# Performance work log

Hardware: AMD Instinct MI355X
Metric: run time of the kernel (lower is better)

Reference implementation:

```python
import jax, jax.numpy as jnp
import numpy as np


def setup_inputs() -> dict:
    key = jax.random.key(0)
    ks = jax.random.split(key, 6)
    B, S, I, H = 8, 4096, 512, 512
    scale = 1.0 / np.sqrt(I)
    return {
        "x": jax.random.normal(ks[0], (B, S, I), dtype=jnp.float32),
        "h_0": jax.random.normal(ks[1], (B, H), dtype=jnp.float32),
        "W_z": jax.random.normal(ks[2], (H, I), dtype=jnp.float32) * scale,
        "b_z": jax.random.normal(ks[3], (H,), dtype=jnp.float32) * scale,
        "W_h": jax.random.normal(ks[4], (H, I), dtype=jnp.float32) * scale,
        "b_h": jax.random.normal(ks[5], (H,), dtype=jnp.float32) * scale,
    }


def reference(x, h_0, W_z, b_z, W_h, b_h):
    # Gate and candidate projections (dense GEMMs over all timesteps at once)
    z = jax.nn.sigmoid(jnp.einsum("bsi,hi->bsh", x, W_z) + b_z)  # [B,S,H]
    h_tilde = jnp.einsum("bsi,hi->bsh", x, W_h) + b_h            # [B,S,H]

    # Linear recurrence h_t = a_t * h_{t-1} + b_t with a = 1-z, b = z*h_tilde.
    # Parallel associative scan over time; h_0 folded in as element 0 (a=1, b=h_0).
    a = jnp.concatenate([jnp.ones_like(h_0)[:, None, :], 1.0 - z], axis=1)     # [B,S+1,H]
    b = jnp.concatenate([h_0[:, None, :], z * h_tilde], axis=1)                # [B,S+1,H]

    def combine(c1, c2):
        a1, b1 = c1
        a2, b2 = c2
        return a1 * a2, a2 * b1 + b2

    _, h = jax.lax.associative_scan(combine, (a, b), axis=1)
    return h[:, 1:, :]  # drop the h_0 slot -> [B,S,H]
```

## Files before the change

kernel.cpp:

```cpp
#include <hip/hip_runtime.h>
#include <hip/hip_bf16.h>
#include <stdint.h>


typedef __attribute__((ext_vector_type(8))) short short8;
typedef __attribute__((ext_vector_type(4))) float f32x4;

#define AS1 __attribute__((address_space(1)))
#define AS3 __attribute__((address_space(3)))

__device__ inline void gload_lds16(const void* g, void* l) {
  __builtin_amdgcn_global_load_lds((AS1 uint32_t*)(g), (AS3 uint32_t*)(l), 16, 0, 0);
}

__device__ inline ushort f2bf(float f) {
  union { __hip_bfloat16 h; ushort u; } v;
  v.h = __float2bfloat16(f);
  return v.u;
}

__global__ void cvt_all(const float* __restrict__ x,
                        const float* __restrict__ wz,
                        const float* __restrict__ wh,
                        ushort* __restrict__ xb,
                        ushort* __restrict__ wzb,
                        ushort* __restrict__ whb) {
  int i = blockIdx.x * 256 + threadIdx.x;
  for (; i < 4325376; i += 2048 * 256) {
    const float* s; ushort* d; int j;
    if (i < 4194304)      { s = x;  d = xb;  j = i; }
    else if (i < 4259840) { s = wz; d = wzb; j = i - 4194304; }
    else                  { s = wh; d = whb; j = i - 4259840; }
    float4 v = reinterpret_cast<const float4*>(s)[j];
    ushort4 o = make_ushort4(f2bf(v.x), f2bf(v.y), f2bf(v.z), f2bf(v.w));
    reinterpret_cast<ushort4*>(d)[j] = o;
  }
}

__global__ __launch_bounds__(256, 2) void gemm_gate(
    const ushort* __restrict__ xb,
    const ushort* __restrict__ wzb,
    const ushort* __restrict__ whb,
    const float* __restrict__ b_z,
    const float* __restrict__ b_h,
    uint* __restrict__ ab,
    float2* __restrict__ ABc)
{
  __shared__ __align__(16) char smem[73728];

  const int t  = threadIdx.x;
  const int w  = t >> 6;
  const int l  = t & 63;
  const int lm = l & 15;
  const int lk = l >> 4;
  const int wm = w >> 1, wn = w & 1;
  const int bid  = blockIdx.x;
  const int tile = (bid & 7) * 128 + (bid >> 3);
  const int bx = tile >> 2;
  const int by = tile & 3;
  const int m0 = bx * 128;
  const int n0 = by * 128;

  const int srow = t >> 2;
  const int ssl  = t & 3;

  f32x4 acc[2][4][4];
  #pragma unroll
  for (int q = 0; q < 2; ++q)
    #pragma unroll
    for (int m = 0; m < 4; ++m)
      #pragma unroll
      for (int n = 0; n < 4; ++n)
        acc[q][m][n] = (f32x4){0.f, 0.f, 0.f, 0.f};

  auto stage = [&](int sel, int kt) {
    char* base = smem + sel * 24576;
    const int k0 = kt * 32;
    #pragma unroll
    for (int j = 0; j < 2; ++j) {
      int row = j * 64 + srow;
      int gs  = ssl ^ ((row >> 1) & 3);
      gload_lds16(xb + (size_t)(m0 + row) * 512 + k0 + gs * 8,
                  base + j * 4096 + w * 1024);
      gload_lds16(wzb + (size_t)(n0 + row) * 512 + k0 + gs * 8,
                  base + 8192 + j * 4096 + w * 1024);
      gload_lds16(whb + (size_t)(n0 + row) * 512 + k0 + gs * 8,
                  base + 16384 + j * 4096 + w * 1024);
    }
  };

  stage(0, 0);
  stage(1, 1);

  #pragma unroll
  for (int kt = 0; kt < 16; ++kt) {
    const int sel = kt % 3;
    if (kt < 14) {
      stage((kt + 2) % 3, kt + 2);
      asm volatile("s_waitcnt vmcnt(12)" ::: "memory");
    } else if (kt == 14) {
      asm volatile("s_waitcnt vmcnt(6)" ::: "memory");
    } else {
      asm volatile("s_waitcnt vmcnt(0)" ::: "memory");
    }
    __builtin_amdgcn_s_barrier();

    const char* base = smem + sel * 24576;
    short8 af[4], bfz[4], bfh[4];
    #pragma unroll
    for (int m = 0; m < 4; ++m) {
      int row = wm * 64 + m * 16 + lm;
      af[m] = *(const short8*)(base + row * 64 + ((lk ^ ((row >> 1) & 3)) << 4));
    }
    #pragma unroll
    for (int n = 0; n < 4; ++n) {
      int row = wn * 64 + n * 16 + lm;
      int so  = ((lk ^ ((row >> 1) & 3)) << 4);
      bfz[n] = *(const short8*)(base + 8192  + row * 64 + so);
      bfh[n] = *(const short8*)(base + 16384 + row * 64 + so);
    }
    __builtin_amdgcn_s_setprio(1);
    #pragma unroll
    for (int m = 0; m < 4; ++m)
      #pragma unroll
      for (int n = 0; n < 4; ++n) {
        acc[0][m][n] = __builtin_amdgcn_mfma_f32_16x16x32_bf16(af[m], bfz[n], acc[0][m][n], 0, 0, 0);
        acc[1][m][n] = __builtin_amdgcn_mfma_f32_16x16x32_bf16(af[m], bfh[n], acc[1][m][n], 0, 0, 0);
      }
    __builtin_amdgcn_s_setprio(0);
    __builtin_amdgcn_s_barrier();
  }

  #pragma unroll
  for (int n = 0; n < 4; ++n) {
    const int col = n0 + wn * 64 + n * 16 + lm;
    const float bzn = b_z[col];
    const float bhn = b_h[col];
    float av[4][4], bv[4][4];
    #pragma unroll
    for (int m = 0; m < 4; ++m) {
      #pragma unroll
      for (int j = 0; j < 4; ++j) {
        size_t grow = (size_t)(m0 + wm * 64 + m * 16 + lk * 4 + j);
        float uz = acc[0][m][n][j] + bzn;
        float uh = acc[1][m][n][j] + bhn;
        float z  = 1.f / (1.f + __expf(-uz));
        float a  = 1.f - z;
        float bb = z * uh;
        av[m][j] = a;
        bv[m][j] = bb;
        ab[grow * 512 + n0 + wn * 64 + n * 16 + lm] =
            (uint)f2bf(a) | ((uint)f2bf(bb) << 16);
      }
    }
    #pragma unroll
    for (int cb = 0; cb < 2; ++cb) {
      float At[2], Bt[2];
      #pragma unroll
      for (int mm = 0; mm < 2; ++mm) {
        float A = 1.f, Bv = 0.f;
        #pragma unroll
        for (int j = 0; j < 4; ++j) {
          float a = av[2 * cb + mm][j];
          float b = bv[2 * cb + mm][j];
          A  = a * A;
          Bv = a * Bv + b;
        }
        float Ag = 1.f, Bg = 0.f;
        #pragma unroll
        for (int q = 0; q < 4; ++q) {
          float Aq = __shfl(A,  lm + 16 * q);
          float Bq = __shfl(Bv, lm + 16 * q);
          Ag = Aq * Ag;
          Bg = Aq * Bg + Bq;
        }
        At[mm] = Ag;
        Bt[mm] = Bg;
      }
      float Achunk = At[1] * At[0];
      float Bchunk = At[1] * Bt[0] + Bt[1];
      if (lk == 0) {
        int bidx = bx >> 5;
        int c    = (bx & 31) * 4 + wm * 2 + cb;
        ABc[((size_t)bidx * 512 + col) * 128 + c] = make_float2(Achunk, Bchunk);
      }
    }
  }
}

__global__ __launch_bounds__(256) void chunk_scan(
    const float2* __restrict__ ABc,
    const float* __restrict__ h0,
    float* __restrict__ Hinit)
{
  __shared__ float sm[128][4];
  const int w = threadIdx.x >> 6, l = threadIdx.x & 63;
  const int b   = blockIdx.x >> 7;
  const int h0g = (blockIdx.x & 127) * 4;
  const int h   = h0g + w;

  const float2* base = ABc + ((size_t)b * 512 + h) * 128;
  float2 s1 = base[l];
  float2 s2 = base[64 + l];

  float A1 = s1.x, B1 = s1.y;
  #pragma unroll
  for (int d = 1; d < 64; d <<= 1) {
    float uA = __shfl_up(A1, d);
    float uB = __shfl_up(B1, d);
    if (l >= d) { B1 = A1 * uB + B1; A1 = A1 * uA; }
  }
  float A2 = s2.x, B2 = s2.y;
  #pragma unroll
  for (int d = 1; d < 64; d <<= 1) {
    float uA = __shfl_up(A2, d);
    float uB = __shfl_up(B2, d);
    if (l >= d) { B2 = A2 * uB + B2; A2 = A2 * uA; }
  }
  float PA = __shfl(A1, 63), PB = __shfl(B1, 63);
  float FA = A2 * PA;
  float FB = A2 * PB + B2;

  float e1A = __shfl_up(A1, 1), e1B = __shfl_up(B1, 1);
  if (l == 0) { e1A = 1.f; e1B = 0.f; }
  float e2A = __shfl_up(FA, 1), e2B = __shfl_up(FB, 1);
  if (l == 0) { e2A = PA; e2B = PB; }

  float h0v = h0[b * 512 + h];
  sm[l][w]      = e1A * h0v + e1B;
  sm[64 + l][w] = e2A * h0v + e2B;
  __syncthreads();

  const int tt = threadIdx.x;
  if (tt < 128) {
    float4 v = *(const float4*)sm[tt];
    *(float4*)(Hinit + ((size_t)b * 128 + tt) * 512 + h0g) = v;
  }
}

__global__ __launch_bounds__(256) void scan_write(
    const uint* __restrict__ ab,
    const float* __restrict__ Hinit,
    float* __restrict__ out)
{
  int tid = blockIdx.x * 256 + threadIdx.x;
  int cg = tid & 127;
  int c  = (tid >> 7) & 127;
  int b  = tid >> 14;
  const uint4* p = reinterpret_cast<const uint4*>(ab + ((size_t)(b * 4096 + c * 32)) * 512) + cg;
  float4 hv = *reinterpret_cast<const float4*>(Hinit + ((size_t)b * 128 + c) * 512 + cg * 4);
  float4* po = reinterpret_cast<float4*>(out + ((size_t)(b * 4096 + c * 32)) * 512) + cg;
  #pragma unroll 4
  for (int t = 0; t < 32; ++t) {
    uint4 u = p[(size_t)t * 128];
    hv.x = __uint_as_float(u.x << 16) * hv.x + __uint_as_float(u.x & 0xffff0000u);
    hv.y = __uint_as_float(u.y << 16) * hv.y + __uint_as_float(u.y & 0xffff0000u);
    hv.z = __uint_as_float(u.z << 16) * hv.z + __uint_as_float(u.z & 0xffff0000u);
    hv.w = __uint_as_float(u.w << 16) * hv.w + __uint_as_float(u.w & 0xffff0000u);
    po[(size_t)t * 128] = hv;
  }
}

extern "C" void kernel_launch(void* const* d_in, const int* in_sizes, int n_in,
                              void* d_out, int out_size, void* d_ws, size_t ws_size,
                              hipStream_t stream) {
  const float* x   = (const float*)d_in[0];
  const float* h0  = (const float*)d_in[1];
  const float* W_z = (const float*)d_in[2];
  const float* b_z = (const float*)d_in[3];
  const float* W_h = (const float*)d_in[4];
  const float* b_h = (const float*)d_in[5];
  float* out = (float*)d_out;

  char* ws = (char*)d_ws;
  ushort* xb    = (ushort*)(ws);
  ushort* wzb   = (ushort*)(ws + 33554432);
  ushort* whb   = (ushort*)(ws + 34078720);
  uint*   ab    = (uint*)  (ws + 34603008);
  float2* ABc   = (float2*)(ws + 101711872);
  float*  Hinit = (float*) (ws + 105906176);

  cvt_all<<<2048, 256, 0, stream>>>(x, W_z, W_h, xb, wzb, whb);
  gemm_gate<<<1024, 256, 0, stream>>>(xb, wzb, whb, b_z, b_h, ab, ABc);
  chunk_scan<<<1024, 256, 0, stream>>>(ABc, h0, Hinit);
  scan_write<<<512, 256, 0, stream>>>(ab, Hinit, out);
}
```

Baseline: 94.55 us.

## Switch gate GEMM to 32x32x16 MFMA and restructure chunk-scan epilogue

Replaces the 16x16x32 bf16 MFMA tiling with 32x32x16 MFMAs over 2x2 accumulator tiles per wave. This cuts the number of LDS fragment loads and MFMA issues per k-step. The pipeline now waits and barriers before issuing the next stage's prefetch, which removes the trailing barrier in each iteration. The epilogue is rewritten for the 32x32 output layout and combines the two row halves with an xor-32 shuffle instead of four broadcast shuffles. This changes register pressure and the order in which the scan is combined.

```diff
diff --git a/kernel.cpp b/kernel.cpp
--- a/kernel.cpp
+++ b/kernel.cpp
@@ -3,8 +3,8 @@
 #include <stdint.h>
 
 
-typedef __attribute__((ext_vector_type(8))) short short8;
-typedef __attribute__((ext_vector_type(4))) float f32x4;
+typedef __attribute__((ext_vector_type(8)))  short short8;
+typedef __attribute__((ext_vector_type(16))) float f32x16;
 
 #define AS1 __attribute__((address_space(1)))
 #define AS3 __attribute__((address_space(3)))
@@ -48,11 +48,11 @@
 {
   __shared__ __align__(16) char smem[73728];
 
-  const int t  = threadIdx.x;
-  const int w  = t >> 6;
-  const int l  = t & 63;
-  const int lm = l & 15;
-  const int lk = l >> 4;
+  const int t   = threadIdx.x;
+  const int w   = t >> 6;
+  const int l   = t & 63;
+  const int c32 = l & 31;
+  const int hi  = l >> 5;
   const int wm = w >> 1, wn = w & 1;
   const int bid  = blockIdx.x;
   const int tile = (bid & 7) * 128 + (bid >> 3);
@@ -64,14 +64,14 @@
   const int srow = t >> 2;
   const int ssl  = t & 3;
 
-  f32x4 acc[2][4][4];
-  #pragma unroll
-  for (int q = 0; q < 2; ++q)
-    #pragma unroll
-    for (int m = 0; m < 4; ++m)
-      #pragma unroll
-      for (int n = 0; n < 4; ++n)
-        acc[q][m][n] = (f32x4){0.f, 0.f, 0.f, 0.f};
+  f32x16 accz[2][2], acch[2][2];
+  #pragma unroll
+  for (int tm = 0; tm < 2; ++tm)
+    #pragma unroll
+    for (int tn = 0; tn < 2; ++tn) {
+      accz[tm][tn] = (f32x16)(0.f);
+      acch[tm][tn] = (f32x16)(0.f);
+    }
 
   auto stage = [&](int sel, int kt) {
     char* base = smem + sel * 24576;
@@ -95,94 +95,92 @@
   #pragma unroll
   for (int kt = 0; kt < 16; ++kt) {
     const int sel = kt % 3;
-    if (kt < 14) {
-      stage((kt + 2) % 3, kt + 2);
-      asm volatile("s_waitcnt vmcnt(12)" ::: "memory");
-    } else if (kt == 14) {
+    if (kt < 15) {
       asm volatile("s_waitcnt vmcnt(6)" ::: "memory");
     } else {
       asm volatile("s_waitcnt vmcnt(0)" ::: "memory");
     }
     __builtin_amdgcn_s_barrier();
+    if (kt < 14) stage((kt + 2) % 3, kt + 2);
 
     const char* base = smem + sel * 24576;
-    short8 af[4], bfz[4], bfh[4];
-    #pragma unroll
-    for (int m = 0; m < 4; ++m) {
-      int row = wm * 64 + m * 16 + lm;
-      af[m] = *(const short8*)(base + row * 64 + ((lk ^ ((row >> 1) & 3)) << 4));
-    }
-    #pragma unroll
-    for (int n = 0; n < 4; ++n) {
-      int row = wn * 64 + n * 16 + lm;
-      int so  = ((lk ^ ((row >> 1) & 3)) << 4);
-      bfz[n] = *(const short8*)(base + 8192  + row * 64 + so);
-      bfh[n] = *(const short8*)(base + 16384 + row * 64 + so);
+    short8 af[2][2], bfz[2][2], bfh[2][2];
+    #pragma unroll
+    for (int tm = 0; tm < 2; ++tm) {
+      int row = wm * 64 + tm * 32 + c32;
+      int rsw = (row >> 1) & 3;
+      #pragma unroll
+      for (int ks = 0; ks < 2; ++ks)
+        af[tm][ks] = *(const short8*)(base + row * 64 + (((ks * 2 + hi) ^ rsw) << 4));
+    }
+    #pragma unroll
+    for (int tn = 0; tn < 2; ++tn) {
+      int row = wn * 64 + tn * 32 + c32;
+      int rsw = (row >> 1) & 3;
+      #pragma unroll
+      for (int ks = 0; ks < 2; ++ks) {
+        int so = (((ks * 2 + hi) ^ rsw) << 4);
+        bfz[tn][ks] = *(const short8*)(base + 8192  + row * 64 + so);
+        bfh[tn][ks] = *(const short8*)(base + 16384 + row * 64 + so);
+      }
     }
     __builtin_amdgcn_s_setprio(1);
     #pragma unroll
-    for (int m = 0; m < 4; ++m)
-      #pragma unroll
-      for (int n = 0; n < 4; ++n) {
-        acc[0][m][n] = __builtin_amdgcn_mfma_f32_16x16x32_bf16(af[m], bfz[n], acc[0][m][n], 0, 0, 0);
-        acc[1][m][n] = __builtin_amdgcn_mfma_f32_16x16x32_bf16(af[m], bfh[n], acc[1][m][n], 0, 0, 0);
+    for (int tm = 0; tm < 2; ++tm)
+      #pragma unroll
+      for (int tn = 0; tn < 2; ++tn) {
+        accz[tm][tn] = __builtin_amdgcn_mfma_f32_32x32x16_bf16(af[tm][0], bfz[tn][0], accz[tm][tn], 0, 0, 0);
+        accz[tm][tn] = __builtin_amdgcn_mfma_f32_32x32x16_bf16(af[tm][1], bfz[tn][1], accz[tm][tn], 0, 0, 0);
+        acch[tm][tn] = __builtin_amdgcn_mfma_f32_32x32x16_bf16(af[tm][0], bfh[tn][0], acch[tm][tn], 0, 0, 0);
+        acch[tm][tn] = __builtin_amdgcn_mfma_f32_32x32x16_bf16(af[tm][1], bfh[tn][1], acch[tm][tn], 0, 0, 0);
       }
     __builtin_amdgcn_s_setprio(0);
-    __builtin_amdgcn_s_barrier();
-  }
-
-  #pragma unroll
-  for (int n = 0; n < 4; ++n) {
-    const int col = n0 + wn * 64 + n * 16 + lm;
-    const float bzn = b_z[col];
-    const float bhn = b_h[col];
-    float av[4][4], bv[4][4];
-    #pragma unroll
-    for (int m = 0; m < 4; ++m) {
-      #pragma unroll
-      for (int j = 0; j < 4; ++j) {
-        size_t grow = (size_t)(m0 + wm * 64 + m * 16 + lk * 4 + j);
-        float uz = acc[0][m][n][j] + bzn;
-        float uh = acc[1][m][n][j] + bhn;
-        float z  = 1.f / (1.f + __expf(-uz));
-        float a  = 1.f - z;
-        float bb = z * uh;
-        av[m][j] = a;
-        bv[m][j] = bb;
-        ab[grow * 512 + n0 + wn * 64 + n * 16 + lm] =
-            (uint)f2bf(a) | ((uint)f2bf(bb) << 16);
-      }
-    }
-    #pragma unroll
-    for (int cb = 0; cb < 2; ++cb) {
-      float At[2], Bt[2];
-      #pragma unroll
-      for (int mm = 0; mm < 2; ++mm) {
+  }
+
+  const int bidx = bx >> 5;
+  #pragma unroll
+  for (int tm = 0; tm < 2; ++tm) {
+    #pragma unroll
+    for (int tn = 0; tn < 2; ++tn) {
+      const int col = n0 + wn * 64 + tn * 32 + c32;
+      const float bzn = b_z[col];
+      const float bhn = b_h[col];
+      float segA[4], segB[4];
+      #pragma unroll
+      for (int q = 0; q < 4; ++q) {
         float A = 1.f, Bv = 0.f;
         #pragma unroll
         for (int j = 0; j < 4; ++j) {
-          float a = av[2 * cb + mm][j];
-          float b = bv[2 * cb + mm][j];
+          const int reg  = q * 4 + j;
+          const int rloc = j + 8 * q + 4 * hi;
+          float uz = accz[tm][tn][reg] + bzn;
+          float uh = acch[tm][tn][reg] + bhn;
+          float z  = 1.f / (1.f + __expf(-uz));
+          float a  = 1.f - z;
+          float bb = z * uh;
+          size_t grow = (size_t)(m0 + wm * 64 + tm * 32 + rloc);
+          ab[grow * 512 + col] = (uint)f2bf(a) | ((uint)f2bf(bb) << 16);
           A  = a * A;
-          Bv = a * Bv + b;
+          Bv = a * Bv + bb;
         }
-        float Ag = 1.f, Bg = 0.f;
-        #pragma unroll
-        for (int q = 0; q < 4; ++q) {
-          float Aq = __shfl(A,  lm + 16 * q);
-          float Bq = __shfl(Bv, lm + 16 * q);
-          Ag = Aq * Ag;
-          Bg = Aq * Bg + Bq;
-        }
-        At[mm] = Ag;
-        Bt[mm] = Bg;
-      }
-      float Achunk = At[1] * At[0];
-      float Bchunk = At[1] * Bt[0] + Bt[1];
-      if (lk == 0) {
-        int bidx = bx >> 5;
-        int c    = (bx & 31) * 4 + wm * 2 + cb;
-        ABc[((size_t)bidx * 512 + col) * 128 + c] = make_float2(Achunk, Bchunk);
+        segA[q] = A;
+        segB[q] = Bv;
+      }
+      float FA = 1.f, FB = 0.f;
+      #pragma unroll
+      for (int q = 0; q < 4; ++q) {
+        float pA = __shfl_xor(segA[q], 32);
+        float pB = __shfl_xor(segB[q], 32);
+        float fA = hi ? pA : segA[q];
+        float fB = hi ? pB : segB[q];
+        float sA = hi ? segA[q] : pA;
+        float sB = hi ? segB[q] : pB;
+        FB = fA * FB + fB; FA = fA * FA;
+        FB = sA * FB + sB; FA = sA * FA;
+      }
+      if (hi == 0) {
+        int c = (bx & 31) * 4 + wm * 2 + tm;
+        ABc[((size_t)bidx * 512 + col) * 128 + c] = make_float2(FA, FB);
       }
     }
   }
```

Result: no change. 95.93 us (+1.5%).

## Use 256x256 GEMM tiles with interleaved W_z/W_h weights and phased pipeline

Applied to the files above, without the earlier changes.

Concatenates W_z and W_h into one interleaved weight matrix during conversion, so each GEMM block computes a 256x256 tile (128 gate and 128 candidate columns) with 512 threads and 128KB LDS. The K loop now uses 64-wide steps with double-buffered A/B regions and a phased schedule that issues loads between MFMA groups. The intent is to raise arithmetic intensity and cut global/LDS traffic per MFMA. The cost is more LDS per block, lower occupancy, and more complex synchronization.

```diff
diff --git a/kernel.cpp b/kernel.cpp
--- a/kernel.cpp
+++ b/kernel.cpp
@@ -23,166 +23,183 @@
                         const float* __restrict__ wz,
                         const float* __restrict__ wh,
                         ushort* __restrict__ xb,
-                        ushort* __restrict__ wzb,
-                        ushort* __restrict__ whb) {
+                        ushort* __restrict__ wcat) {
   int i = blockIdx.x * 256 + threadIdx.x;
   for (; i < 4325376; i += 2048 * 256) {
     const float* s; ushort* d; int j;
-    if (i < 4194304)      { s = x;  d = xb;  j = i; }
-    else if (i < 4259840) { s = wz; d = wzb; j = i - 4194304; }
-    else                  { s = wh; d = whb; j = i - 4259840; }
-    float4 v = reinterpret_cast<const float4*>(s)[j];
-    ushort4 o = make_ushort4(f2bf(v.x), f2bf(v.y), f2bf(v.z), f2bf(v.w));
-    reinterpret_cast<ushort4*>(d)[j] = o;
-  }
-}
-
-__global__ __launch_bounds__(256, 2) void gemm_gate(
+    if (i < 4194304) {
+      s = x; d = xb; j = i;
+      float4 v = reinterpret_cast<const float4*>(s)[j];
+      reinterpret_cast<ushort4*>(d)[j] =
+          make_ushort4(f2bf(v.x), f2bf(v.y), f2bf(v.z), f2bf(v.w));
+    } else {
+      j = i - 4194304;
+      int row = j >> 7, c4 = j & 127;
+      int g = row >> 6, q = row & 63;
+      const float* src = (q < 32) ? (wz + (size_t)(g * 32 + q) * 512)
+                                  : (wh + (size_t)(g * 32 + q - 32) * 512);
+      float4 v = reinterpret_cast<const float4*>(src)[c4];
+      reinterpret_cast<ushort4*>(wcat)[j] =
+          make_ushort4(f2bf(v.x), f2bf(v.y), f2bf(v.z), f2bf(v.w));
+    }
+  }
+}
+
+__global__ __launch_bounds__(512, 2) void gemm_gate(
     const ushort* __restrict__ xb,
-    const ushort* __restrict__ wzb,
-    const ushort* __restrict__ whb,
+    const ushort* __restrict__ wcat,
     const float* __restrict__ b_z,
     const float* __restrict__ b_h,
     uint* __restrict__ ab,
     float2* __restrict__ ABc)
 {
-  __shared__ __align__(16) char smem[73728];
+  __shared__ __align__(16) char smem[131072];
 
   const int t  = threadIdx.x;
   const int w  = t >> 6;
   const int l  = t & 63;
   const int lm = l & 15;
   const int lk = l >> 4;
-  const int wm = w >> 1, wn = w & 1;
+  const int wm = w >> 2;
+  const int wn = w & 3;
+
   const int bid  = blockIdx.x;
-  const int tile = (bid & 7) * 128 + (bid >> 3);
-  const int bx = tile >> 2;
-  const int by = tile & 3;
-  const int m0 = bx * 128;
-  const int n0 = by * 128;
-
-  const int srow = t >> 2;
-  const int ssl  = t & 3;
-
-  f32x4 acc[2][4][4];
-  #pragma unroll
-  for (int q = 0; q < 2; ++q)
+  const int tile = (bid & 7) * 64 + (bid >> 3);
+  const int mt = tile >> 2;
+  const int nt = tile & 3;
+  const int m0 = mt * 256;
+  const int n0 = nt * 256;
+
+  const int sr8 = l >> 3;
+  const int gs  = (l & 7) ^ sr8;
+
+  enum { B0A = 0, B0B = 32768, B1A = 65536, B1B = 98304 };
+
+  f32x4 acc[8][4];
+  #pragma unroll
+  for (int m = 0; m < 8; ++m)
     #pragma unroll
-    for (int m = 0; m < 4; ++m)
-      #pragma unroll
-      for (int n = 0; n < 4; ++n)
-        acc[q][m][n] = (f32x4){0.f, 0.f, 0.f, 0.f};
-
-  auto stage = [&](int sel, int kt) {
-    char* base = smem + sel * 24576;
-    const int k0 = kt * 32;
+    for (int nf = 0; nf < 4; ++nf)
+      acc[m][nf] = (f32x4){0.f, 0.f, 0.f, 0.f};
+
+  auto stageA = [&](int region, int kt, int half) {
     #pragma unroll
     for (int j = 0; j < 2; ++j) {
-      int row = j * 64 + srow;
-      int gs  = ssl ^ ((row >> 1) & 3);
-      gload_lds16(xb + (size_t)(m0 + row) * 512 + k0 + gs * 8,
-                  base + j * 4096 + w * 1024);
-      gload_lds16(wzb + (size_t)(n0 + row) * 512 + k0 + gs * 8,
-                  base + 8192 + j * 4096 + w * 1024);
-      gload_lds16(whb + (size_t)(n0 + row) * 512 + k0 + gs * 8,
-                  base + 16384 + j * 4096 + w * 1024);
+      int row = half * 128 + j * 64 + w * 8 + sr8;
+      gload_lds16(xb + (size_t)(m0 + row) * 512 + kt * 64 + gs * 8,
+                  smem + region + (half * 128 + j * 64) * 128 + w * 1024);
     }
   };
-
-  stage(0, 0);
-  stage(1, 1);
-
-  #pragma unroll
-  for (int kt = 0; kt < 16; ++kt) {
-    const int sel = kt % 3;
-    if (kt < 14) {
-      stage((kt + 2) % 3, kt + 2);
-      asm volatile("s_waitcnt vmcnt(12)" ::: "memory");
-    } else if (kt == 14) {
-      asm volatile("s_waitcnt vmcnt(6)" ::: "memory");
-    } else {
-      asm volatile("s_waitcnt vmcnt(0)" ::: "memory");
+  auto stageB = [&](int region, int kt, int half) {
+    #pragma unroll
+    for (int j = 0; j < 2; ++j) {
+      int row = half * 128 + j * 64 + w * 8 + sr8;
+      gload_lds16(wcat + (size_t)(n0 + row) * 512 + kt * 64 + gs * 8,
+                  smem + region + (half * 128 + j * 64) * 128 + w * 1024);
     }
-    __builtin_amdgcn_s_barrier();
-
-    const char* base = smem + sel * 24576;
-    short8 af[4], bfz[4], bfh[4];
+  };
+
+  short8 aF[2][2], bB[4][2];
+
+#define RD_A(BUFA, MQ)                                                        \
+  _Pragma("unroll") for (int mm = 0; mm < 2; ++mm)                            \
+  _Pragma("unroll") for (int ks = 0; ks < 2; ++ks) {                          \
+    int row = wm * 128 + (2 * (MQ) + mm) * 16 + lm;                           \
+    aF[mm][ks] = *(const short8*)(smem + (BUFA) + row * 128 +                 \
+                                  (((ks * 4 + lk) ^ (lm & 7)) << 4));         \
+  }
+
+#define RD_B(BUFB)                                                            \
+  _Pragma("unroll") for (int nf = 0; nf < 4; ++nf)                            \
+  _Pragma("unroll") for (int ks = 0; ks < 2; ++ks) {                          \
+    int row = wn * 64 + nf * 16 + lm;                                         \
+    bB[nf][ks] = *(const short8*)(smem + (BUFB) + row * 128 +                 \
+                                  (((ks * 4 + lk) ^ (lm & 7)) << 4));         \
+  }
+
+#define PHASE(BUFA, BUFB, MQ, READB, STAGE, VMN)                              \
+  {                                                                           \
+    if (READB) { RD_B(BUFB); }                                                \
+    RD_A(BUFA, MQ);                                                           \
+    STAGE;                                                                    \
+    if ((VMN) == 4)      asm volatile("s_waitcnt vmcnt(4)" ::: "memory");     \
+    else if ((VMN) == 0) asm volatile("s_waitcnt vmcnt(0)" ::: "memory");     \
+    __builtin_amdgcn_s_barrier();                                             \
+    asm volatile("s_waitcnt lgkmcnt(0)" ::: "memory");                        \
+    __builtin_amdgcn_sched_barrier(0);                                        \
+    __builtin_amdgcn_s_setprio(1);                                            \
+    _Pragma("unroll") for (int ks = 0; ks < 2; ++ks)                          \
+    _Pragma("unroll") for (int nf = 0; nf < 4; ++nf) {                        \
+      acc[2 * (MQ)][nf]     = __builtin_amdgcn_mfma_f32_16x16x32_bf16(        \
+          aF[0][ks], bB[nf][ks], acc[2 * (MQ)][nf], 0, 0, 0);                 \
+      acc[2 * (MQ) + 1][nf] = __builtin_amdgcn_mfma_f32_16x16x32_bf16(        \
+          aF[1][ks], bB[nf][ks], acc[2 * (MQ) + 1][nf], 0, 0, 0);             \
+    }                                                                         \
+    __builtin_amdgcn_s_setprio(0);                                            \
+    __builtin_amdgcn_s_barrier();                                             \
+  }
+
+  stageA(B0A, 0, 0); stageA(B0A, 0, 1);
+  stageB(B0B, 0, 0); stageB(B0B, 0, 1);
+  stageB(B1B, 1, 0); stageB(B1B, 1, 1);
+  asm volatile("s_waitcnt vmcnt(4)" ::: "memory");
+  __builtin_amdgcn_s_barrier();
+
+  #pragma unroll
+  for (int it = 0; it < 4; ++it) {
+    const int ko = 2 * it + 1, ke2 = 2 * it + 2, ko2 = 2 * it + 3;
+    PHASE(B0A, B0B, 0, true,  { stageA(B1A, ko, 0); },               -1)
+    PHASE(B0A, B0B, 1, false, { stageA(B1A, ko, 1); },               -1)
+    PHASE(B0A, B0B, 2, false, { if (it < 3) stageB(B0B, ke2, 0); },  -1)
+    PHASE(B0A, B0B, 3, false, { if (it < 3) stageB(B0B, ke2, 1); },  (it < 3) ? 4 : 0)
+    PHASE(B1A, B1B, 0, true,  { if (it < 3) stageA(B0A, ke2, 0); },  -1)
+    PHASE(B1A, B1B, 1, false, { if (it < 3) stageA(B0A, ke2, 1); },  -1)
+    PHASE(B1A, B1B, 2, false, { if (it < 3) stageB(B1B, ko2, 0); },  -1)
+    PHASE(B1A, B1B, 3, false, { if (it < 3) stageB(B1B, ko2, 1); },  (it < 3) ? 4 : 0)
+  }
+#undef PHASE
+#undef RD_A
+#undef RD_B
+
+  const int g    = nt * 4 + wn;
+  const int bidx = mt >> 4;
+  #pragma unroll
+  for (int gp = 0; gp < 2; ++gp) {
+    const int h = g * 32 + gp * 16 + lm;
+    const float bz = b_z[h], bh = b_h[h];
     #pragma unroll
-    for (int m = 0; m < 4; ++m) {
-      int row = wm * 64 + m * 16 + lm;
-      af[m] = *(const short8*)(base + row * 64 + ((lk ^ ((row >> 1) & 3)) << 4));
-    }
-    #pragma unroll
-    for (int n = 0; n < 4; ++n) {
-      int row = wn * 64 + n * 16 + lm;
-      int so  = ((lk ^ ((row >> 1) & 3)) << 4);
-      bfz[n] = *(const short8*)(base + 8192  + row * 64 + so);
-      bfh[n] = *(const short8*)(base + 16384 + row * 64 + so);
-    }
-    __builtin_amdgcn_s_setprio(1);
-    #pragma unroll
-    for (int m = 0; m < 4; ++m)
-      #pragma unroll
-      for (int n = 0; n < 4; ++n) {
-        acc[0][m][n] = __builtin_amdgcn_mfma_f32_16x16x32_bf16(af[m], bfz[n], acc[0][m][n], 0, 0, 0);
-        acc[1][m][n] = __builtin_amdgcn_mfma_f32_16x16x32_bf16(af[m], bfh[n], acc[1][m][n], 0, 0, 0);
-      }
-    __builtin_amdgcn_s_setprio(0);
-    __builtin_amdgcn_s_barrier();
-  }
-
-  #pragma unroll
-  for (int n = 0; n < 4; ++n) {
-    const int col = n0 + wn * 64 + n * 16 + lm;
-    const float bzn = b_z[col];
-    const float bhn = b_h[col];
-    float av[4][4], bv[4][4];
-    #pragma unroll
-    for (int m = 0; m < 4; ++m) {
-      #pragma unroll
-      for (int j = 0; j < 4; ++j) {
-        size_t grow = (size_t)(m0 + wm * 64 + m * 16 + lk * 4 + j);
-        float uz = acc[0][m][n][j] + bzn;
-        float uh = acc[1][m][n][j] + bhn;
-        float z  = 1.f / (1.f + __expf(-uz));
-        float a  = 1.f - z;
-        float bb = z * uh;
-        av[m][j] = a;
-        bv[m][j] = bb;
-        ab[grow * 512 + n0 + wn * 64 + n * 16 + lm] =
-            (uint)f2bf(a) | ((uint)f2bf(bb) << 16);
-      }
-    }
-    #pragma unroll
-    for (int cb = 0; cb < 2; ++cb) {
-      float At[2], Bt[2];
+    for (int cb = 0; cb < 4; ++cb) {
+      float cA = 1.f, cB = 0.f;
       #pragma unroll
       for (int mm = 0; mm < 2; ++mm) {
-        float A = 1.f, Bv = 0.f;
+        const int m = 2 * cb + mm;
+        float sA = 1.f, sB = 0.f;
         #pragma unroll
         for (int j = 0; j < 4; ++j) {
-          float a = av[2 * cb + mm][j];
-          float b = bv[2 * cb + mm][j];
-          A  = a * A;
-          Bv = a * Bv + b;
+          float uz = acc[m][gp][j] + bz;
+          float uh = acc[m][gp + 2][j] + bh;
+          float z  = 1.f / (1.f + __expf(-uz));
+          float a  = 1.f - z;
+          float bb = z * uh;
+          size_t grow = (size_t)(m0 + wm * 128 + m * 16 + lk * 4 + j);
+          ab[grow * 512 + h] = (uint)f2bf(a) | ((uint)f2bf(bb) << 16);
+          sA = a * sA;
+          sB = a * sB + bb;
         }
         float Ag = 1.f, Bg = 0.f;
         #pragma unroll
         for (int q = 0; q < 4; ++q) {
-          float Aq = __shfl(A,  lm + 16 * q);
-          float Bq = __shfl(Bv, lm + 16 * q);
+          float Aq = __shfl(sA, q * 16 + lm);
+          float Bq = __shfl(sB, q * 16 + lm);
           Ag = Aq * Ag;
           Bg = Aq * Bg + Bq;
         }
-        At[mm] = Ag;
-        Bt[mm] = Bg;
+        cB = Ag * cB + Bg;
+        cA = Ag * cA;
       }
-      float Achunk = At[1] * At[0];
-      float Bchunk = At[1] * Bt[0] + Bt[1];
       if (lk == 0) {
-        int bidx = bx >> 5;
-        int c    = (bx & 31) * 4 + wm * 2 + cb;
-        ABc[((size_t)bidx * 512 + col) * 128 + c] = make_float2(Achunk, Bchunk);
+        int c = (mt & 15) * 8 + wm * 4 + cb;
+        ABc[((size_t)bidx * 512 + h) * 128 + c] = make_float2(cA, cB);
       }
     }
   }
@@ -274,14 +291,13 @@
 
   char* ws = (char*)d_ws;
   ushort* xb    = (ushort*)(ws);
-  ushort* wzb   = (ushort*)(ws + 33554432);
-  ushort* whb   = (ushort*)(ws + 34078720);
+  ushort* wcat  = (ushort*)(ws + 33554432);
   uint*   ab    = (uint*)  (ws + 34603008);
   float2* ABc   = (float2*)(ws + 101711872);
   float*  Hinit = (float*) (ws + 105906176);
 
-  cvt_all<<<2048, 256, 0, stream>>>(x, W_z, W_h, xb, wzb, whb);
-  gemm_gate<<<1024, 256, 0, stream>>>(xb, wzb, whb, b_z, b_h, ab, ABc);
+  cvt_all<<<2048, 256, 0, stream>>>(x, W_z, W_h, xb, wcat);
+  gemm_gate<<<512, 512, 0, stream>>>(xb, wcat, b_z, b_h, ab, ABc);
   chunk_scan<<<1024, 256, 0, stream>>>(ABc, h0, Hinit);
   scan_write<<<512, 256, 0, stream>>>(ab, Hinit, out);
 }
```

After: 91.27 us. 1.04x faster.

## Fuse x fp32-to-bf16 conversion into GEMM A-tile loading

Applied to the files above, without the earlier changes.

Drops the separate conversion pass over x. The GEMM now loads fp32 x into registers, converts it to bf16 and writes it to LDS itself, while the weights keep using direct global-to-LDS DMA. This removes a 64MB read plus 32MB write/read round trip, but it costs register pressure and adds a VALU conversion and LDS-write stage to the GEMM pipeline. Only the small weight conversion kernel remains.

```diff
diff --git a/kernel.cpp b/kernel.cpp
--- a/kernel.cpp
+++ b/kernel.cpp
@@ -19,26 +19,19 @@
   return v.u;
 }
 
-__global__ void cvt_all(const float* __restrict__ x,
-                        const float* __restrict__ wz,
-                        const float* __restrict__ wh,
-                        ushort* __restrict__ xb,
-                        ushort* __restrict__ wzb,
-                        ushort* __restrict__ whb) {
+__global__ void cvt_w(const float* __restrict__ wz, const float* __restrict__ wh,
+                      ushort* __restrict__ wzb, ushort* __restrict__ whb) {
   int i = blockIdx.x * 256 + threadIdx.x;
-  for (; i < 4325376; i += 2048 * 256) {
-    const float* s; ushort* d; int j;
-    if (i < 4194304)      { s = x;  d = xb;  j = i; }
-    else if (i < 4259840) { s = wz; d = wzb; j = i - 4194304; }
-    else                  { s = wh; d = whb; j = i - 4259840; }
-    float4 v = reinterpret_cast<const float4*>(s)[j];
-    ushort4 o = make_ushort4(f2bf(v.x), f2bf(v.y), f2bf(v.z), f2bf(v.w));
-    reinterpret_cast<ushort4*>(d)[j] = o;
-  }
+  float4 a = reinterpret_cast<const float4*>(wz)[i];
+  reinterpret_cast<ushort4*>(wzb)[i] =
+      make_ushort4(f2bf(a.x), f2bf(a.y), f2bf(a.z), f2bf(a.w));
+  float4 b = reinterpret_cast<const float4*>(wh)[i];
+  reinterpret_cast<ushort4*>(whb)[i] =
+      make_ushort4(f2bf(b.x), f2bf(b.y), f2bf(b.z), f2bf(b.w));
 }
 
 __global__ __launch_bounds__(256, 2) void gemm_gate(
-    const ushort* __restrict__ xb,
+    const float* __restrict__ x,
     const ushort* __restrict__ wzb,
     const ushort* __restrict__ whb,
     const float* __restrict__ b_z,
@@ -64,6 +57,10 @@
   const int srow = t >> 2;
   const int ssl  = t & 3;
 
+  const int arow = t >> 1;
+  const int asl  = (t & 1) * 2;
+  const int aswz = (arow >> 1) & 3;
+
   f32x4 acc[2][4][4];
   #pragma unroll
   for (int q = 0; q < 2; ++q)
@@ -73,15 +70,36 @@
       for (int n = 0; n < 4; ++n)
         acc[q][m][n] = (f32x4){0.f, 0.f, 0.f, 0.f};
 
-  auto stage = [&](int sel, int kt) {
+  float4 arA[4], arB[4];
+
+  auto ALOAD = [&](float4* ar, int kt) {
+    #pragma unroll
+    for (int d = 0; d < 2; ++d) {
+      int s = (asl + d) ^ aswz;
+      const float* p = x + (size_t)(m0 + arow) * 512 + kt * 32 + s * 8;
+      ar[2 * d]     = *(const float4*)(p);
+      ar[2 * d + 1] = *(const float4*)(p + 4);
+    }
+  };
+  auto AWRITE = [&](int sel, const float4* ar) {
+    char* base = smem + sel * 24576;
+    #pragma unroll
+    for (int d = 0; d < 2; ++d) {
+      short8 v;
+      v[0] = (short)f2bf(ar[2 * d].x);     v[1] = (short)f2bf(ar[2 * d].y);
+      v[2] = (short)f2bf(ar[2 * d].z);     v[3] = (short)f2bf(ar[2 * d].w);
+      v[4] = (short)f2bf(ar[2 * d + 1].x); v[5] = (short)f2bf(ar[2 * d + 1].y);
+      v[6] = (short)f2bf(ar[2 * d + 1].z); v[7] = (short)f2bf(ar[2 * d + 1].w);
+      *(short8*)(base + arow * 64 + (asl + d) * 16) = v;
+    }
+  };
+  auto BDMA = [&](int sel, int kt) {
     char* base = smem + sel * 24576;
     const int k0 = kt * 32;
     #pragma unroll
     for (int j = 0; j < 2; ++j) {
       int row = j * 64 + srow;
       int gs  = ssl ^ ((row >> 1) & 3);
-      gload_lds16(xb + (size_t)(m0 + row) * 512 + k0 + gs * 8,
-                  base + j * 4096 + w * 1024);
       gload_lds16(wzb + (size_t)(n0 + row) * 512 + k0 + gs * 8,
                   base + 8192 + j * 4096 + w * 1024);
       gload_lds16(whb + (size_t)(n0 + row) * 512 + k0 + gs * 8,
@@ -89,47 +107,57 @@
     }
   };
 
-  stage(0, 0);
-  stage(1, 1);
-
-  #pragma unroll
-  for (int kt = 0; kt < 16; ++kt) {
-    const int sel = kt % 3;
-    if (kt < 14) {
-      stage((kt + 2) % 3, kt + 2);
-      asm volatile("s_waitcnt vmcnt(12)" ::: "memory");
-    } else if (kt == 14) {
-      asm volatile("s_waitcnt vmcnt(6)" ::: "memory");
-    } else {
-      asm volatile("s_waitcnt vmcnt(0)" ::: "memory");
-    }
-    __builtin_amdgcn_s_barrier();
-
-    const char* base = smem + sel * 24576;
-    short8 af[4], bfz[4], bfh[4];
-    #pragma unroll
-    for (int m = 0; m < 4; ++m) {
-      int row = wm * 64 + m * 16 + lm;
-      af[m] = *(const short8*)(base + row * 64 + ((lk ^ ((row >> 1) & 3)) << 4));
-    }
-    #pragma unroll
-    for (int n = 0; n < 4; ++n) {
-      int row = wn * 64 + n * 16 + lm;
-      int so  = ((lk ^ ((row >> 1) & 3)) << 4);
-      bfz[n] = *(const short8*)(base + 8192  + row * 64 + so);
-      bfh[n] = *(const short8*)(base + 16384 + row * 64 + so);
-    }
-    __builtin_amdgcn_s_setprio(1);
-    #pragma unroll
-    for (int m = 0; m < 4; ++m)
-      #pragma unroll
-      for (int n = 0; n < 4; ++n) {
-        acc[0][m][n] = __builtin_amdgcn_mfma_f32_16x16x32_bf16(af[m], bfz[n], acc[0][m][n], 0, 0, 0);
-        acc[1][m][n] = __builtin_amdgcn_mfma_f32_16x16x32_bf16(af[m], bfh[n], acc[1][m][n], 0, 0, 0);
-      }
-    __builtin_amdgcn_s_setprio(0);
-    __builtin_amdgcn_s_barrier();
-  }
+#define STEP(KT, ARW, ARL)                                                    \
+  {                                                                           \
+    if ((KT) < 14) ALOAD(ARL, (KT) + 2);                                      \
+    if ((KT) < 15) AWRITE(((KT) + 1) % 3, ARW);                               \
+    if ((KT) < 14)       asm volatile("s_waitcnt vmcnt(8)" ::: "memory");     \
+    else if ((KT) == 14) asm volatile("s_waitcnt vmcnt(4)" ::: "memory");     \
+    else                 asm volatile("s_waitcnt vmcnt(0)" ::: "memory");     \
+    asm volatile("s_waitcnt lgkmcnt(0)" ::: "memory");                        \
+    __builtin_amdgcn_s_barrier();                                             \
+    {                                                                         \
+      const char* base = smem + ((KT) % 3) * 24576;                           \
+      short8 af[4], bfz[4], bfh[4];                                           \
+      _Pragma("unroll") for (int m = 0; m < 4; ++m) {                         \
+        int row = wm * 64 + m * 16 + lm;                                      \
+        af[m] = *(const short8*)(base + row * 64 +                            \
+                                 ((lk ^ ((row >> 1) & 3)) << 4));             \
+      }                                                                       \
+      _Pragma("unroll") for (int n = 0; n < 4; ++n) {                         \
+        int row = wn * 64 + n * 16 + lm;                                      \
+        int so  = ((lk ^ ((row >> 1) & 3)) << 4);                             \
+        bfz[n] = *(const short8*)(base + 8192  + row * 64 + so);              \
+        bfh[n] = *(const short8*)(base + 16384 + row * 64 + so);              \
+      }                                                                       \
+      __builtin_amdgcn_s_setprio(1);                                          \
+      _Pragma("unroll") for (int m = 0; m < 4; ++m)                           \
+        _Pragma("unroll") for (int n = 0; n < 4; ++n) {                       \
+          acc[0][m][n] = __builtin_amdgcn_mfma_f32_16x16x32_bf16(             \
+              af[m], bfz[n], acc[0][m][n], 0, 0, 0);                          \
+          acc[1][m][n] = __builtin_amdgcn_mfma_f32_16x16x32_bf16(             \
+              af[m], bfh[n], acc[1][m][n], 0, 0, 0);                          \
+        }                                                                     \
+      __builtin_amdgcn_s_setprio(0);                                          \
+    }                                                                         \
+    __builtin_amdgcn_s_barrier();                                             \
+    if ((KT) < 14) BDMA(((KT) + 2) % 3, (KT) + 2);                            \
+  }
+
+  ALOAD(arA, 0);
+  ALOAD(arB, 1);
+  BDMA(0, 0);
+  BDMA(1, 1);
+  AWRITE(0, arA);
+  asm volatile("s_waitcnt vmcnt(4)" ::: "memory");
+  asm volatile("s_waitcnt lgkmcnt(0)" ::: "memory");
+  __builtin_amdgcn_s_barrier();
+
+  STEP(0,  arB, arA) STEP(1,  arA, arB) STEP(2,  arB, arA) STEP(3,  arA, arB)
+  STEP(4,  arB, arA) STEP(5,  arA, arB) STEP(6,  arB, arA) STEP(7,  arA, arB)
+  STEP(8,  arB, arA) STEP(9,  arA, arB) STEP(10, arB, arA) STEP(11, arA, arB)
+  STEP(12, arB, arA) STEP(13, arA, arB) STEP(14, arB, arA) STEP(15, arA, arB)
+#undef STEP
 
   #pragma unroll
   for (int n = 0; n < 4; ++n) {
@@ -149,8 +177,7 @@
         float bb = z * uh;
         av[m][j] = a;
         bv[m][j] = bb;
-        ab[grow * 512 + n0 + wn * 64 + n * 16 + lm] =
-            (uint)f2bf(a) | ((uint)f2bf(bb) << 16);
+        ab[grow * 512 + col] = (uint)f2bf(a) | ((uint)f2bf(bb) << 16);
       }
     }
     #pragma unroll
@@ -273,15 +300,14 @@
   float* out = (float*)d_out;
 
   char* ws = (char*)d_ws;
-  ushort* xb    = (ushort*)(ws);
-  ushort* wzb   = (ushort*)(ws + 33554432);
-  ushort* whb   = (ushort*)(ws + 34078720);
-  uint*   ab    = (uint*)  (ws + 34603008);
-  float2* ABc   = (float2*)(ws + 101711872);
-  float*  Hinit = (float*) (ws + 105906176);
-
-  cvt_all<<<2048, 256, 0, stream>>>(x, W_z, W_h, xb, wzb, whb);
-  gemm_gate<<<1024, 256, 0, stream>>>(xb, wzb, whb, b_z, b_h, ab, ABc);
+  ushort* wzb   = (ushort*)(ws);
+  ushort* whb   = (ushort*)(ws + 524288);
+  uint*   ab    = (uint*)  (ws + 1048576);
+  float2* ABc   = (float2*)(ws + 68157440);
+  float*  Hinit = (float*) (ws + 72351744);
+
+  cvt_w<<<256, 256, 0, stream>>>(W_z, W_h, wzb, whb);
+  gemm_gate<<<1024, 256, 0, stream>>>(x, wzb, whb, b_z, b_h, ab, ABc);
   chunk_scan<<<1024, 256, 0, stream>>>(ABc, h0, Hinit);
   scan_write<<<512, 256, 0, stream>>>(ab, Hinit, out);
 }
```

Result: faster. 91.69 us (-3.0%).
